# Optimization experiments

Hardware: AMD Instinct MI355X
Metric: run time of the kernel (lower is better)

The kernel has to match this reference:

```python
import jax, jax.numpy as jnp
import numpy as np

N = 100000   # nodes
E = 1600000  # edges (avg degree 16)
G = 512      # graphs in batch
IN = 96      # in_channels
H = 128      # hidden_channels
C = 100      # num_classes
ED = 8       # edge_dim
L = 4        # num_layers
EPS_LN = 1e-5


def setup_inputs() -> dict:
    key = jax.random.key(0)
    ks = jax.random.split(key, 24)
    s = 0.05
    d = {
        "x": jax.random.normal(ks[0], (N, IN), jnp.float32),
        "edge_index": jax.random.randint(ks[1], (2, E), 0, N, jnp.int32),
        "batch": jnp.sort(jax.random.randint(ks[2], (N,), 0, G, jnp.int32)),
        "edge_attr": jax.random.normal(ks[3], (E, ED), jnp.float32),
        # edge encoder MLP: Linear(ED,H) -> ReLU -> Linear(H,1)
        "ee_W1": jax.random.normal(ks[4], (ED, H), jnp.float32) * s,
        "ee_b1": jnp.zeros((H,), jnp.float32),
        "ee_W2": jax.random.normal(ks[5], (H, 1), jnp.float32) * s,
        "ee_b2": jnp.zeros((1,), jnp.float32),
        # GCNConv weights (PyG: lin without bias, bias added after aggregation)
        "W0": jax.random.normal(ks[6], (IN, H), jnp.float32) * s,
        "cb0": jnp.zeros((H,), jnp.float32),
        "W1": jax.random.normal(ks[7], (H, H), jnp.float32) * s,
        "cb1": jnp.zeros((H,), jnp.float32),
        "W2": jax.random.normal(ks[8], (H, H), jnp.float32) * s,
        "cb2": jnp.zeros((H,), jnp.float32),
        "W3": jax.random.normal(ks[9], (H, H), jnp.float32) * s,
        "cb3": jnp.zeros((H,), jnp.float32),
        # LayerNorm params
        "g0": jnp.ones((H,), jnp.float32), "be0": jnp.zeros((H,), jnp.float32),
        "g1": jnp.ones((H,), jnp.float32), "be1": jnp.zeros((H,), jnp.float32),
        "g2": jnp.ones((H,), jnp.float32), "be2": jnp.zeros((H,), jnp.float32),
        "g3": jnp.ones((H,), jnp.float32), "be3": jnp.zeros((H,), jnp.float32),
        # residual projection for layer 0 only (IN != H)
        "res_W": jax.random.normal(ks[10], (IN, H), jnp.float32) * s,
        "res_b": jnp.zeros((H,), jnp.float32),
        # head: Linear(2H,H) -> ReLU -> Linear(H,C)
        "hW1": jax.random.normal(ks[11], (2 * H, H), jnp.float32) * s,
        "hb1": jnp.zeros((H,), jnp.float32),
        "hW2": jax.random.normal(ks[12], (H, C), jnp.float32) * s,
        "hb2": jnp.zeros((C,), jnp.float32),
    }
    return d


def _layer_norm(h, g, b):
    mu = jnp.mean(h, axis=-1, keepdims=True)
    var = jnp.mean(jnp.square(h - mu), axis=-1, keepdims=True)
    return g * (h - mu) / jnp.sqrt(var + EPS_LN) + b


def reference(x, edge_index, batch, edge_attr,
              ee_W1, ee_b1, ee_W2, ee_b2,
              W0, cb0, W1, cb1, W2, cb2, W3, cb3,
              g0, be0, g1, be1, g2, be2, g3, be3,
              res_W, res_b, hW1, hb1, hW2, hb2):
    row, col = edge_index[0], edge_index[1]

    # edge weight = softplus(MLP(edge_attr)) + 1e-4  -> [E]
    eh = jax.nn.relu(edge_attr @ ee_W1 + ee_b1)
    ew = jax.nn.softplus((eh @ ee_W2 + ee_b2)[:, 0]) + 1e-4

    # add self loops with weight 1 (PyG GCNConv default)
    loops = jnp.arange(N, dtype=row.dtype)
    row_sl = jnp.concatenate([row, loops])
    col_sl = jnp.concatenate([col, loops])
    ew_sl = jnp.concatenate([ew, jnp.ones((N,), ew.dtype)])

    # symmetric normalization: D^-1/2 A D^-1/2 (deg over target index)
    deg = jax.ops.segment_sum(ew_sl, col_sl, num_segments=N)
    dis = jnp.where(deg > 0, jax.lax.rsqrt(deg), 0.0)
    norm = dis[row_sl] * ew_sl * dis[col_sl]  # [E+N]

    def conv(h, W, b):
        hw = h @ W                                   # [N,H]
        msg = hw[row_sl] * norm[:, None]             # [E+N,H]
        return jax.ops.segment_sum(msg, col_sl, num_segments=N) + b

    Ws = [W0, W1, W2, W3]
    cbs = [cb0, cb1, cb2, cb3]
    gs = [g0, g1, g2, g3]
    bes = [be0, be1, be2, be3]

    hidden = []
    cur = x
    for i in range(L):
        h = conv(cur, Ws[i], cbs[i])
        h = _layer_norm(h, gs[i], bes[i])
        res = cur @ res_W + res_b if i == 0 else cur
        h = jax.nn.relu(h + res)
        # dropout: eval mode -> identity
        hidden.append(h)
        cur = h
    xm = jnp.mean(jnp.stack(hidden, axis=0), axis=0)  # [N,H]

    # meanmax pooling over graphs
    counts = jax.ops.segment_sum(jnp.ones((N,), xm.dtype), batch, num_segments=G)
    gmean = jax.ops.segment_sum(xm, batch, num_segments=G) / jnp.maximum(counts, 1.0)[:, None]
    gmax = jax.ops.segment_max(xm, batch, num_segments=G)
    gmax = jnp.where(jnp.isfinite(gmax), gmax, 0.0)
    g = jnp.concatenate([gmean, gmax], axis=-1)       # [G,2H]

    # head (dropout identity in eval)
    return jax.nn.relu(g @ hW1 + hb1) @ hW2 + hb2     # [G,C]
```

## Files before the change

### kernel.cpp

```cpp
#include <hip/hip_runtime.h>
#include <hip/hip_fp16.h>
#include <math.h>

#define NN 100000
#define EE 1600000
#define GB 512
#define INC 96
#define HH 128
#define CC 100
#define MAXD 64
#define BUCKB 9
#define NBUK 196
#define CAPB 10240
#define EB 4096

typedef __bf16 bf16x8 __attribute__((ext_vector_type(8)));
typedef _Float16 f16x8 __attribute__((ext_vector_type(8)));
typedef float f32x4 __attribute__((ext_vector_type(4)));

__device__ __forceinline__ float unpack_w_f32(unsigned v) {
    return __half2float(__ushort_as_half((unsigned short)(v & 0x7FFFu)));
}
__device__ __forceinline__ __half2 unpack_w_h2(unsigned v) {
    __half h = __ushort_as_half((unsigned short)(v & 0x7FFFu));
    return __halves2half2(h, h);
}

__global__ __launch_bounds__(256) void k_cast(const float* __restrict__ src, __half* __restrict__ dst, int n4) {
    int i = blockIdx.x * 256 + threadIdx.x;
    if (i >= n4) return;
    float4 v = *(const float4*)&src[(size_t)i * 4];
    __half2 a = __floats2half2_rn(v.x, v.y);
    __half2 b = __floats2half2_rn(v.z, v.w);
    *(__half2*)&dst[(size_t)i * 4]     = a;
    *(__half2*)&dst[(size_t)i * 4 + 2] = b;
}

__global__ __launch_bounds__(256) void k_prep_weights(
    const float* __restrict__ W0, const float* __restrict__ resW,
    const float* __restrict__ W1m, const float* __restrict__ W2m, const float* __restrict__ W3m,
    __half* __restrict__ wt0, __half* __restrict__ wtR,
    __half* __restrict__ wt1, __half* __restrict__ wt2, __half* __restrict__ wt3)
{
    int idx = blockIdx.x * 256 + threadIdx.x;
    const float* src; __half* dst; int K, base;
    if (idx < 12288)      { src = W0;   dst = wt0; K = 96;  base = 0; }
    else if (idx < 24576) { src = resW; dst = wtR; K = 96;  base = 12288; }
    else if (idx < 40960) { src = W1m;  dst = wt1; K = 128; base = 24576; }
    else if (idx < 57344) { src = W2m;  dst = wt2; K = 128; base = 40960; }
    else if (idx < 73728) { src = W3m;  dst = wt3; K = 128; base = 57344; }
    else return;
    int l = idx - base;
    int k = l >> 7, n = l & 127;
    dst[(size_t)n * K + k] = __float2half(src[l]);
}

__global__ __launch_bounds__(512) void k_prep_w1(const float* __restrict__ W1, __bf16* __restrict__ w1f) {
    int tid = threadIdx.x;
    int t = tid >> 6, lane = tid & 63;
    int ln15 = lane & 15, quad = lane >> 4;
    bf16x8 v = {};
    if (quad == 0) {
#pragma unroll
        for (int j = 0; j < 8; ++j) v[j] = (__bf16)W1[j * 128 + t * 16 + ln15];
    }
    *(bf16x8*)&w1f[(size_t)(t * 64 + lane) * 8] = v;
}

__global__ __launch_bounds__(256) void k_edge_mlp_mfma(
    const float* __restrict__ ea,
    const __bf16* __restrict__ w1f, const float* __restrict__ b1,
    const float* __restrict__ W2, const float* __restrict__ b2,
    __half* __restrict__ ew)
{
    __shared__ float sDot[128];
    int tid = threadIdx.x, wva = tid >> 6, lane = tid & 63;
    int ln15 = lane & 15, quad = lane >> 4;
    int ebase = blockIdx.x * 128 + wva * 32;

    bf16x8 bfr[8];
#pragma unroll
    for (int t = 0; t < 8; ++t) bfr[t] = *(const bf16x8*)&w1f[(size_t)(t * 64 + lane) * 8];

    bf16x8 a0 = {}, a1 = {};
    if (quad == 0) {
        const float* p0 = &ea[(size_t)(ebase + ln15) * 8];
        float4 u0 = *(const float4*)p0, u1 = *(const float4*)(p0 + 4);
        a0[0] = (__bf16)u0.x; a0[1] = (__bf16)u0.y; a0[2] = (__bf16)u0.z; a0[3] = (__bf16)u0.w;
        a0[4] = (__bf16)u1.x; a0[5] = (__bf16)u1.y; a0[6] = (__bf16)u1.z; a0[7] = (__bf16)u1.w;
        const float* p1 = &ea[(size_t)(ebase + 16 + ln15) * 8];
        float4 w0 = *(const float4*)p1, w1v = *(const float4*)(p1 + 4);
        a1[0] = (__bf16)w0.x; a1[1] = (__bf16)w0.y; a1[2] = (__bf16)w0.z; a1[3] = (__bf16)w0.w;
        a1[4] = (__bf16)w1v.x; a1[5] = (__bf16)w1v.y; a1[6] = (__bf16)w1v.z; a1[7] = (__bf16)w1v.w;
    }

    f32x4 d0 = {0.f, 0.f, 0.f, 0.f}, d1 = {0.f, 0.f, 0.f, 0.f};
#pragma unroll
    for (int t = 0; t < 8; ++t) {
        f32x4 z = {0.f, 0.f, 0.f, 0.f};
        f32x4 c0 = __builtin_amdgcn_mfma_f32_16x16x32_bf16(a0, bfr[t], z, 0, 0, 0);
        f32x4 c1 = __builtin_amdgcn_mfma_f32_16x16x32_bf16(a1, bfr[t], z, 0, 0, 0);
        int col = t * 16 + ln15;
        float b1v = b1[col], w2v = W2[col];
#pragma unroll
        for (int r = 0; r < 4; ++r) {
            float v0 = fmaxf(c0[r] + b1v, 0.0f);
            float v1 = fmaxf(c1[r] + b1v, 0.0f);
            d0[r] = fmaf(v0, w2v, d0[r]);
            d1[r] = fmaf(v1, w2v, d1[r]);
        }
    }
#pragma unroll
    for (int o = 1; o < 16; o <<= 1) {
#pragma unroll
        for (int r = 0; r < 4; ++r) {
            d0[r] += __shfl_xor(d0[r], o, 64);
            d1[r] += __shfl_xor(d1[r], o, 64);
        }
    }
    if (ln15 == 0) {
#pragma unroll
        for (int r = 0; r < 4; ++r) {
            sDot[wva * 32 + quad * 4 + r]      = d0[r];
            sDot[wva * 32 + 16 + quad * 4 + r] = d1[r];
        }
    }
    __syncthreads();
    if (tid < 128) {
        int e = blockIdx.x * 128 + tid;
        float x = sDot[tid] + b2[0];
        float sp = (x > 20.0f) ? x : log1pf(expf(x));
        ew[e] = __float2half(sp + 1e-4f);
    }
}

__global__ __launch_bounds__(256) void k_split(const int* __restrict__ ei, const __half* __restrict__ ew,
                                               int* __restrict__ cntB, uint2* __restrict__ barr) {
    __shared__ unsigned hist[NBUK];
    __shared__ unsigned gbase[NBUK];
    __shared__ unsigned short rloc[EB];
    int tid = threadIdx.x;
    for (int b = tid; b < NBUK; b += 256) hist[b] = 0;
    __syncthreads();
    int e0 = blockIdx.x * EB;
#pragma unroll
    for (int j = 0; j < EB / 256; ++j) {
        int e = e0 + j * 256 + tid;
        if (e < EE) {
            int c = ei[EE + e];
            rloc[j * 256 + tid] = (unsigned short)atomicAdd(&hist[c >> BUCKB], 1u);
        }
    }
    __syncthreads();
    for (int b = tid; b < NBUK; b += 256)
        gbase[b] = (hist[b] > 0) ? (unsigned)atomicAdd(&cntB[b], (int)hist[b]) : 0u;
    __syncthreads();
#pragma unroll
    for (int j = 0; j < EB / 256; ++j) {
        int e = e0 + j * 256 + tid;
        if (e < EE) {
            int c = ei[EE + e];
            int b = c >> BUCKB;
            unsigned pos = gbase[b] + rloc[j * 256 + tid];
            if (pos < CAPB) {
                unsigned hb = (unsigned)__half_as_ushort(ew[e]) & 0x7FFFu;
                barr[(size_t)b * CAPB + pos] = make_uint2(((unsigned)c << 15) | hb, (unsigned)ei[e]);
            }
        }
    }
}

__global__ __launch_bounds__(256) void k_build(const int* __restrict__ cntB, const uint2* __restrict__ barr,
                                               unsigned* __restrict__ epack, int* __restrict__ cnt,
                                               float* __restrict__ dis) {
    __shared__ unsigned ncnt[512];
    __shared__ float ndeg[512];
    int tid = threadIdx.x, b = blockIdx.x;
    for (int i = tid; i < 512; i += 256) { ncnt[i] = 0; ndeg[i] = 0.0f; }
    __syncthreads();
    int n0 = b << BUCKB;
    int m = cntB[b]; if (m > CAPB) m = CAPB;
    for (int i = tid; i < m; i += 256) {
        uint2 rec = barr[(size_t)b * CAPB + i];
        int c = (int)(rec.x >> 15);
        int cl = c - n0;
        unsigned rank = atomicAdd(&ncnt[cl], 1u);
        if (rank < MAXD) epack[(size_t)c * MAXD + rank] = (rec.y << 15) | (rec.x & 0x7FFFu);
        atomicAdd(&ndeg[cl], unpack_w_f32(rec.x));
    }
    __syncthreads();
    int nn = NN - n0; if (nn > 512) nn = 512;
    for (int i = tid; i < nn; i += 256) {
        unsigned cc = ncnt[i]; if (cc > MAXD) cc = MAXD;
        cnt[n0 + i] = (int)cc;
        dis[n0 + i] = rsqrtf(1.0f + ndeg[i]);
    }
}

__global__ __launch_bounds__(256) void k_norm(const int* __restrict__ cnt, const float* __restrict__ dis,
                                              unsigned* __restrict__ epack, int n) {
    int wv = threadIdx.x >> 6, lane = threadIdx.x & 63;
    int i = blockIdx.x * 4 + wv;
    if (i >= n) return;
    float dc = dis[i];
    if (lane < cnt[i]) {
        unsigned v = epack[(size_t)i * MAXD + lane];
        float wn = dis[v >> 15] * unpack_w_f32(v) * dc;
        unsigned hb = (unsigned)__half_as_ushort(__float2half(wn)) & 0x7FFFu;
        epack[(size_t)i * MAXD + lane] = (v & 0xFFFF8000u) | hb;
    }
}

__global__ __launch_bounds__(256) void k_gemm_f16(
    const __half* __restrict__ A, const __half* __restrict__ Bt,
    const float* __restrict__ bias, __half* __restrict__ C, int M, int K)
{
    int tid = threadIdx.x;
    int wv = tid >> 6, lane = tid & 63;
    int ln15 = lane & 15, quad = lane >> 4;
    int m0 = blockIdx.x * 64;
    int n0 = wv * 32;
    f32x4 acc[4][2];
#pragma unroll
    for (int mt = 0; mt < 4; ++mt)
#pragma unroll
        for (int nt = 0; nt < 2; ++nt) acc[mt][nt] = (f32x4){0.f, 0.f, 0.f, 0.f};

    int rowm[4];
#pragma unroll
    for (int mt = 0; mt < 4; ++mt) {
        int r = m0 + mt * 16 + ln15;
        rowm[mt] = r < M ? r : M - 1;
    }
    for (int kc = 0; kc < K; kc += 32) {
        f16x8 af[4], bfr[2];
#pragma unroll
        for (int mt = 0; mt < 4; ++mt)
            af[mt] = *(const f16x8*)&A[(size_t)rowm[mt] * K + kc + quad * 8];
#pragma unroll
        for (int nt = 0; nt < 2; ++nt)
            bfr[nt] = *(const f16x8*)&Bt[(size_t)(n0 + nt * 16 + ln15) * K + kc + quad * 8];
#pragma unroll
        for (int mt = 0; mt < 4; ++mt)
#pragma unroll
            for (int nt = 0; nt < 2; ++nt)
                acc[mt][nt] = __builtin_amdgcn_mfma_f32_16x16x32_f16(af[mt], bfr[nt], acc[mt][nt], 0, 0, 0);
    }
#pragma unroll
    for (int nt = 0; nt < 2; ++nt) {
        int col = n0 + nt * 16 + ln15;
        float bv = bias ? bias[col] : 0.0f;
#pragma unroll
        for (int mt = 0; mt < 4; ++mt) {
#pragma unroll
            for (int r = 0; r < 4; ++r) {
                int row = m0 + mt * 16 + quad * 4 + r;
                if (row < M) C[(size_t)row * 128 + col] = __float2half(acc[mt][nt][r] + bv);
            }
        }
    }
}

__global__ __launch_bounds__(256) void k_agg_ln(
    const __half* __restrict__ hw, const float* __restrict__ dis,
    const int* __restrict__ cnt, const unsigned* __restrict__ epack,
    const float* __restrict__ cb, const float* __restrict__ gam,
    const float* __restrict__ bet, const __half* __restrict__ res,
    __half* __restrict__ out, int n)
{
    int wv = threadIdx.x >> 6;
    int lane = threadIdx.x & 63;
    int i = blockIdx.x * 4 + wv;
    if (i >= n) return;
    float di = dis[i];
    float sn = di * di;
    __half2 own = *(const __half2*)&hw[(size_t)i * HH + lane * 2];
    __half hsn = __float2half(sn);
    __half2 acc = __hmul2(own, __halves2half2(hsn, hsn));
    int cn = cnt[i];
    const unsigned* ebase = &epack[(size_t)i * MAXD];
    int k = 0;
    for (; k + 8 <= cn; k += 8) {
        uint4 q0 = *(const uint4*)&ebase[k];
        uint4 q1 = *(const uint4*)&ebase[k + 4];
        __half2 v0 = *(const __half2*)&hw[(size_t)(q0.x >> 15) * HH + lane * 2];
        __half2 v1 = *(const __half2*)&hw[(size_t)(q0.y >> 15) * HH + lane * 2];
        __half2 v2 = *(const __half2*)&hw[(size_t)(q0.z >> 15) * HH + lane * 2];
        __half2 v3 = *(const __half2*)&hw[(size_t)(q0.w >> 15) * HH + lane * 2];
        __half2 v4 = *(const __half2*)&hw[(size_t)(q1.x >> 15) * HH + lane * 2];
        __half2 v5 = *(const __half2*)&hw[(size_t)(q1.y >> 15) * HH + lane * 2];
        __half2 v6 = *(const __half2*)&hw[(size_t)(q1.z >> 15) * HH + lane * 2];
        __half2 v7 = *(const __half2*)&hw[(size_t)(q1.w >> 15) * HH + lane * 2];
        acc = __hfma2(v0, unpack_w_h2(q0.x), acc);
        acc = __hfma2(v1, unpack_w_h2(q0.y), acc);
        acc = __hfma2(v2, unpack_w_h2(q0.z), acc);
        acc = __hfma2(v3, unpack_w_h2(q0.w), acc);
        acc = __hfma2(v4, unpack_w_h2(q1.x), acc);
        acc = __hfma2(v5, unpack_w_h2(q1.y), acc);
        acc = __hfma2(v6, unpack_w_h2(q1.z), acc);
        acc = __hfma2(v7, unpack_w_h2(q1.w), acc);
    }
    for (; k < cn; ++k) {
        unsigned e = ebase[k];
        __half2 v = *(const __half2*)&hw[(size_t)(e >> 15) * HH + lane * 2];
        acc = __hfma2(v, unpack_w_h2(e), acc);
    }
    float2 af = __half22float2(acc);
    float2 cbv = *(const float2*)&cb[lane * 2];
    af.x += cbv.x; af.y += cbv.y;
    float s1 = af.x + af.y;
    float s2 = af.x * af.x + af.y * af.y;
#pragma unroll
    for (int o = 32; o > 0; o >>= 1) {
        s1 += __shfl_xor(s1, o, 64);
        s2 += __shfl_xor(s2, o, 64);
    }
    float mean = s1 * (1.0f / HH);
    float var = fmaxf(s2 * (1.0f / HH) - mean * mean, 0.0f);
    float rstd = rsqrtf(var + 1e-5f);
    float2 gv = *(const float2*)&gam[lane * 2];
    float2 bv = *(const float2*)&bet[lane * 2];
    float2 rv = __half22float2(*(const __half2*)&res[(size_t)i * HH + lane * 2]);
    float hx = fmaxf(fmaf(gv.x, (af.x - mean) * rstd, bv.x) + rv.x, 0.0f);
    float hy = fmaxf(fmaf(gv.y, (af.y - mean) * rstd, bv.y) + rv.y, 0.0f);
    *(__half2*)&out[(size_t)i * HH + lane * 2] = __floats2half2_rn(hx, hy);
}

__global__ __launch_bounds__(512) void k_pool(
    const __half* __restrict__ l0, const __half* __restrict__ l1,
    const __half* __restrict__ l2, const __half* __restrict__ l3,
    const int* __restrict__ batch, float* __restrict__ gbuf, int n)
{
    __shared__ float ssum[8][128];
    __shared__ float smax[8][128];
    int g = blockIdx.x, tid = threadIdx.x;
    int grp = tid >> 6, lane = tid & 63;
    int lo = 0, hi = n;
    while (lo < hi) { int m = (lo + hi) >> 1; if (batch[m] < g) lo = m + 1; else hi = m; }
    int start = lo;
    lo = start; hi = n;
    while (lo < hi) { int m = (lo + hi) >> 1; if (batch[m] < g + 1) lo = m + 1; else hi = m; }
    int end = lo;
    float sx = 0.0f, sy = 0.0f, mx = -INFINITY, my = -INFINITY;
    for (int nd = start + grp; nd < end; nd += 8) {
        size_t off = (size_t)nd * HH + lane * 2;
        float2 v0 = __half22float2(*(const __half2*)&l0[off]);
        float2 v1 = __half22float2(*(const __half2*)&l1[off]);
        float2 v2 = __half22float2(*(const __half2*)&l2[off]);
        float2 v3 = __half22float2(*(const __half2*)&l3[off]);
        float vx = (v0.x + v1.x + v2.x + v3.x) * 0.25f;
        float vy = (v0.y + v1.y + v2.y + v3.y) * 0.25f;
        sx += vx; sy += vy;
        mx = fmaxf(mx, vx); my = fmaxf(my, vy);
    }
    ssum[grp][lane * 2] = sx; ssum[grp][lane * 2 + 1] = sy;
    smax[grp][lane * 2] = mx; smax[grp][lane * 2 + 1] = my;
    __syncthreads();
    if (tid < 128) {
        float s = 0.0f, m = -INFINITY;
#pragma unroll
        for (int j = 0; j < 8; ++j) {
            s += ssum[j][tid];
            m = fmaxf(m, smax[j][tid]);
        }
        int cntg = end - start;
        gbuf[(size_t)g * 256 + tid] = s / fmaxf((float)cntg, 1.0f);
        gbuf[(size_t)g * 256 + 128 + tid] = (cntg > 0) ? m : 0.0f;
    }
}

__global__ __launch_bounds__(128) void k_head(const float* __restrict__ gbuf,
                                              const float* __restrict__ hW1, const float* __restrict__ hb1,
                                              const float* __restrict__ hW2, const float* __restrict__ hb2,
                                              float* __restrict__ out) {
    __shared__ __align__(16) float sg[256];
    __shared__ __align__(16) float sh[128];
    int g = blockIdx.x, t = threadIdx.x;
    sg[t] = gbuf[(size_t)g * 256 + t];
    sg[t + 128] = gbuf[(size_t)g * 256 + 128 + t];
    __syncthreads();
    float h = hb1[t];
    for (int k = 0; k < 256; ++k) h = fmaf(sg[k], hW1[(size_t)k * 128 + t], h);
    sh[t] = fmaxf(h, 0.0f);
    __syncthreads();
    if (t < 100) {
        float o = hb2[t];
        for (int k = 0; k < 128; ++k) o = fmaf(sh[k], hW2[(size_t)k * 100 + t], o);
        out[(size_t)g * 100 + t] = o;
    }
}

extern "C" void kernel_launch(void* const* d_in, const int* in_sizes, int n_in,
                              void* d_out, int out_size, void* d_ws, size_t ws_size,
                              hipStream_t stream) {
    const float* x     = (const float*)d_in[0];
    const int*   ei    = (const int*)d_in[1];
    const int*   batch = (const int*)d_in[2];
    const float* ea    = (const float*)d_in[3];
    const float* eeW1  = (const float*)d_in[4];
    const float* eeb1  = (const float*)d_in[5];
    const float* eeW2  = (const float*)d_in[6];
    const float* eeb2  = (const float*)d_in[7];
    const float* W[4]  = {(const float*)d_in[8], (const float*)d_in[10], (const float*)d_in[12], (const float*)d_in[14]};
    const float* cb[4] = {(const float*)d_in[9], (const float*)d_in[11], (const float*)d_in[13], (const float*)d_in[15]};
    const float* gm[4] = {(const float*)d_in[16], (const float*)d_in[18], (const float*)d_in[20], (const float*)d_in[22]};
    const float* be[4] = {(const float*)d_in[17], (const float*)d_in[19], (const float*)d_in[21], (const float*)d_in[23]};
    const float* resW  = (const float*)d_in[24];
    const float* resb  = (const float*)d_in[25];
    const float* hW1   = (const float*)d_in[26];
    const float* hb1   = (const float*)d_in[27];
    const float* hW2   = (const float*)d_in[28];
    const float* hb2   = (const float*)d_in[29];
    float* out = (float*)d_out;

    char* w = (char*)d_ws;
    auto alloc = [&](size_t bytes) { void* p = w; w += (bytes + 255) & ~(size_t)255; return p; };
    __half*   ew     = (__half*)  alloc((size_t)EE * 2);
    float*    dis    = (float*)   alloc((size_t)NN * 4);
    int*      cnt    = (int*)     alloc((size_t)NN * 4);
    int*      cntB   = (int*)     alloc((size_t)NBUK * 4);
    uint2*    barr   = (uint2*)   alloc((size_t)NBUK * CAPB * 8);
    unsigned* epack  = (unsigned*)alloc((size_t)NN * MAXD * 4);
    __half*   xb     = (__half*)  alloc((size_t)NN * INC * 2);
    __half*   hw     = (__half*)  alloc((size_t)NN * HH * 2);
    __half*   lout[4];
    for (int i = 0; i < 4; ++i) lout[i] = (__half*)alloc((size_t)NN * HH * 2);
    float*    gbuf   = (float*)   alloc((size_t)GB * 256 * 4);
    __half*   wt0    = (__half*)  alloc((size_t)INC * HH * 2);
    __half*   wtR    = (__half*)  alloc((size_t)INC * HH * 2);
    __half*   wt1    = (__half*)  alloc((size_t)HH * HH * 2);
    __half*   wt2    = (__half*)  alloc((size_t)HH * HH * 2);
    __half*   wt3    = (__half*)  alloc((size_t)HH * HH * 2);
    __bf16*   w1f    = (__bf16*)  alloc((size_t)8 * 64 * 8 * 2);
    __half*   wtc[4] = {wt0, wt1, wt2, wt3};
    __half*   res0   = lout[1];

    int nblkEdge = EE / 128;
    int nblkSplit = (EE + EB - 1) / EB;
    int nblkGemm = (NN + 63) / 64;
    int nblkCast = (NN * INC / 4 + 255) / 256;

    hipMemsetAsync(cntB, 0, (size_t)NBUK * 4, stream);
    k_cast<<<nblkCast, 256, 0, stream>>>(x, xb, NN * INC / 4);
    k_prep_weights<<<288, 256, 0, stream>>>(W[0], resW, W[1], W[2], W[3], wt0, wtR, wt1, wt2, wt3);
    k_prep_w1<<<1, 512, 0, stream>>>(eeW1, w1f);
    k_edge_mlp_mfma<<<nblkEdge, 256, 0, stream>>>(ea, w1f, eeb1, eeW2, eeb2, ew);
    k_split<<<nblkSplit, 256, 0, stream>>>(ei, ew, cntB, barr);
    k_build<<<NBUK, 256, 0, stream>>>(cntB, barr, epack, cnt, dis);
    k_norm<<<(NN + 3) / 4, 256, 0, stream>>>(cnt, dis, epack, NN);

    k_gemm_f16<<<nblkGemm, 256, 0, stream>>>(xb, wt0, nullptr, hw, NN, INC);
    k_gemm_f16<<<nblkGemm, 256, 0, stream>>>(xb, wtR, resb, res0, NN, INC);
    k_agg_ln<<<(NN + 3) / 4, 256, 0, stream>>>(hw, dis, cnt, epack,
                                               cb[0], gm[0], be[0], res0, lout[0], NN);
    for (int l = 1; l < 4; ++l) {
        k_gemm_f16<<<nblkGemm, 256, 0, stream>>>(lout[l - 1], wtc[l], nullptr, hw, NN, HH);
        k_agg_ln<<<(NN + 3) / 4, 256, 0, stream>>>(hw, dis, cnt, epack,
                                                   cb[l], gm[l], be[l], lout[l - 1], lout[l], NN);
    }

    k_pool<<<GB, 512, 0, stream>>>(lout[0], lout[1], lout[2], lout[3], batch, gbuf, NN);
    k_head<<<GB, 128, 0, stream>>>(gbuf, hW1, hb1, hW2, hb2, out);
}
```

Measured before the change: 774.2 us.

## Fuse prep, dual layer-0 GEMMs, pool+head; split agg accumulators

```diff
diff --git a/kernel.cpp b/kernel.cpp
--- a/kernel.cpp
+++ b/kernel.cpp
@@ -36,13 +36,28 @@
     *(__half2*)&dst[(size_t)i * 4 + 2] = b;
 }
 
-__global__ __launch_bounds__(256) void k_prep_weights(
+__global__ __launch_bounds__(512) void k_prep(
     const float* __restrict__ W0, const float* __restrict__ resW,
     const float* __restrict__ W1m, const float* __restrict__ W2m, const float* __restrict__ W3m,
+    const float* __restrict__ eeW1,
     __half* __restrict__ wt0, __half* __restrict__ wtR,
-    __half* __restrict__ wt1, __half* __restrict__ wt2, __half* __restrict__ wt3)
+    __half* __restrict__ wt1, __half* __restrict__ wt2, __half* __restrict__ wt3,
+    __bf16* __restrict__ w1f)
 {
-    int idx = blockIdx.x * 256 + threadIdx.x;
+    int tid = threadIdx.x;
+    if (blockIdx.x == 288) {
+        int t = tid >> 6, lane = tid & 63;
+        int ln15 = lane & 15, quad = lane >> 4;
+        bf16x8 v = {};
+        if (quad == 0) {
+#pragma unroll
+            for (int j = 0; j < 8; ++j) v[j] = (__bf16)eeW1[j * 128 + t * 16 + ln15];
+        }
+        *(bf16x8*)&w1f[(size_t)(t * 64 + lane) * 8] = v;
+        return;
+    }
+    if (tid >= 256) return;
+    int idx = blockIdx.x * 256 + tid;
     const float* src; __half* dst; int K, base;
     if (idx < 12288)      { src = W0;   dst = wt0; K = 96;  base = 0; }
     else if (idx < 24576) { src = resW; dst = wtR; K = 96;  base = 12288; }
@@ -53,18 +68,6 @@
     int l = idx - base;
     int k = l >> 7, n = l & 127;
     dst[(size_t)n * K + k] = __float2half(src[l]);
-}
-
-__global__ __launch_bounds__(512) void k_prep_w1(const float* __restrict__ W1, __bf16* __restrict__ w1f) {
-    int tid = threadIdx.x;
-    int t = tid >> 6, lane = tid & 63;
-    int ln15 = lane & 15, quad = lane >> 4;
-    bf16x8 v = {};
-    if (quad == 0) {
-#pragma unroll
-        for (int j = 0; j < 8; ++j) v[j] = (__bf16)W1[j * 128 + t * 16 + ln15];
-    }
-    *(bf16x8*)&w1f[(size_t)(t * 64 + lane) * 8] = v;
 }
 
 __global__ __launch_bounds__(256) void k_edge_mlp_mfma(
@@ -256,6 +259,65 @@
             for (int r = 0; r < 4; ++r) {
                 int row = m0 + mt * 16 + quad * 4 + r;
                 if (row < M) C[(size_t)row * 128 + col] = __float2half(acc[mt][nt][r] + bv);
+            }
+        }
+    }
+}
+
+__global__ __launch_bounds__(256) void k_gemm_dual(
+    const __half* __restrict__ A, const __half* __restrict__ Bt1, const __half* __restrict__ Bt2,
+    const float* __restrict__ bias2, __half* __restrict__ C1, __half* __restrict__ C2, int M, int K)
+{
+    int tid = threadIdx.x;
+    int wv = tid >> 6, lane = tid & 63;
+    int ln15 = lane & 15, quad = lane >> 4;
+    int m0 = blockIdx.x * 64;
+    int n0 = wv * 32;
+    f32x4 acc1[4][2], acc2[4][2];
+#pragma unroll
+    for (int mt = 0; mt < 4; ++mt)
+#pragma unroll
+        for (int nt = 0; nt < 2; ++nt) {
+            acc1[mt][nt] = (f32x4){0.f, 0.f, 0.f, 0.f};
+            acc2[mt][nt] = (f32x4){0.f, 0.f, 0.f, 0.f};
+        }
+    int rowm[4];
+#pragma unroll
+    for (int mt = 0; mt < 4; ++mt) {
+        int r = m0 + mt * 16 + ln15;
+        rowm[mt] = r < M ? r : M - 1;
+    }
+    for (int kc = 0; kc < K; kc += 32) {
+        f16x8 af[4], bf1[2], bf2[2];
+#pragma unroll
+        for (int mt = 0; mt < 4; ++mt)
+            af[mt] = *(const f16x8*)&A[(size_t)rowm[mt] * K + kc + quad * 8];
+#pragma unroll
+        for (int nt = 0; nt < 2; ++nt) {
+            bf1[nt] = *(const f16x8*)&Bt1[(size_t)(n0 + nt * 16 + ln15) * K + kc + quad * 8];
+            bf2[nt] = *(const f16x8*)&Bt2[(size_t)(n0 + nt * 16 + ln15) * K + kc + quad * 8];
+        }
+#pragma unroll
+        for (int mt = 0; mt < 4; ++mt)
+#pragma unroll
+            for (int nt = 0; nt < 2; ++nt) {
+                acc1[mt][nt] = __builtin_amdgcn_mfma_f32_16x16x32_f16(af[mt], bf1[nt], acc1[mt][nt], 0, 0, 0);
+                acc2[mt][nt] = __builtin_amdgcn_mfma_f32_16x16x32_f16(af[mt], bf2[nt], acc2[mt][nt], 0, 0, 0);
+            }
+    }
+#pragma unroll
+    for (int nt = 0; nt < 2; ++nt) {
+        int col = n0 + nt * 16 + ln15;
+        float bv2 = bias2[col];
+#pragma unroll
+        for (int mt = 0; mt < 4; ++mt) {
+#pragma unroll
+            for (int r = 0; r < 4; ++r) {
+                int row = m0 + mt * 16 + quad * 4 + r;
+                if (row < M) {
+                    C1[(size_t)row * 128 + col] = __float2half(acc1[mt][nt][r]);
+                    C2[(size_t)row * 128 + col] = __float2half(acc2[mt][nt][r] + bv2);
+                }
             }
         }
     }
@@ -276,7 +338,8 @@
     float sn = di * di;
     __half2 own = *(const __half2*)&hw[(size_t)i * HH + lane * 2];
     __half hsn = __float2half(sn);
-    __half2 acc = __hmul2(own, __halves2half2(hsn, hsn));
+    __half2 acca = __hmul2(own, __halves2half2(hsn, hsn));
+    __half2 accb = __halves2half2(__float2half(0.0f), __float2half(0.0f));
     int cn = cnt[i];
     const unsigned* ebase = &epack[(size_t)i * MAXD];
     int k = 0;
@@ -291,20 +354,21 @@
         __half2 v5 = *(const __half2*)&hw[(size_t)(q1.y >> 15) * HH + lane * 2];
         __half2 v6 = *(const __half2*)&hw[(size_t)(q1.z >> 15) * HH + lane * 2];
         __half2 v7 = *(const __half2*)&hw[(size_t)(q1.w >> 15) * HH + lane * 2];
-        acc = __hfma2(v0, unpack_w_h2(q0.x), acc);
-        acc = __hfma2(v1, unpack_w_h2(q0.y), acc);
-        acc = __hfma2(v2, unpack_w_h2(q0.z), acc);
-        acc = __hfma2(v3, unpack_w_h2(q0.w), acc);
-        acc = __hfma2(v4, unpack_w_h2(q1.x), acc);
-        acc = __hfma2(v5, unpack_w_h2(q1.y), acc);
-        acc = __hfma2(v6, unpack_w_h2(q1.z), acc);
-        acc = __hfma2(v7, unpack_w_h2(q1.w), acc);
+        acca = __hfma2(v0, unpack_w_h2(q0.x), acca);
+        accb = __hfma2(v4, unpack_w_h2(q1.x), accb);
+        acca = __hfma2(v1, unpack_w_h2(q0.y), acca);
+        accb = __hfma2(v5, unpack_w_h2(q1.y), accb);
+        acca = __hfma2(v2, unpack_w_h2(q0.z), acca);
+        accb = __hfma2(v6, unpack_w_h2(q1.z), accb);
+        acca = __hfma2(v3, unpack_w_h2(q0.w), acca);
+        accb = __hfma2(v7, unpack_w_h2(q1.w), accb);
     }
     for (; k < cn; ++k) {
         unsigned e = ebase[k];
         __half2 v = *(const __half2*)&hw[(size_t)(e >> 15) * HH + lane * 2];
-        acc = __hfma2(v, unpack_w_h2(e), acc);
-    }
+        acca = __hfma2(v, unpack_w_h2(e), acca);
+    }
+    __half2 acc = __hadd2(acca, accb);
     float2 af = __half22float2(acc);
     float2 cbv = *(const float2*)&cb[lane * 2];
     af.x += cbv.x; af.y += cbv.y;
@@ -326,13 +390,18 @@
     *(__half2*)&out[(size_t)i * HH + lane * 2] = __floats2half2_rn(hx, hy);
 }
 
-__global__ __launch_bounds__(512) void k_pool(
+__global__ __launch_bounds__(512) void k_pool_head(
     const __half* __restrict__ l0, const __half* __restrict__ l1,
     const __half* __restrict__ l2, const __half* __restrict__ l3,
-    const int* __restrict__ batch, float* __restrict__ gbuf, int n)
+    const int* __restrict__ batch,
+    const float* __restrict__ hW1, const float* __restrict__ hb1,
+    const float* __restrict__ hW2, const float* __restrict__ hb2,
+    float* __restrict__ out, int n)
 {
     __shared__ float ssum[8][128];
     __shared__ float smax[8][128];
+    __shared__ __align__(16) float sg[256];
+    __shared__ __align__(16) float sh[128];
     int g = blockIdx.x, tid = threadIdx.x;
     int grp = tid >> 6, lane = tid & 63;
     int lo = 0, hi = n;
@@ -364,29 +433,20 @@
             m = fmaxf(m, smax[j][tid]);
         }
         int cntg = end - start;
-        gbuf[(size_t)g * 256 + tid] = s / fmaxf((float)cntg, 1.0f);
-        gbuf[(size_t)g * 256 + 128 + tid] = (cntg > 0) ? m : 0.0f;
-    }
-}
-
-__global__ __launch_bounds__(128) void k_head(const float* __restrict__ gbuf,
-                                              const float* __restrict__ hW1, const float* __restrict__ hb1,
-                                              const float* __restrict__ hW2, const float* __restrict__ hb2,
-                                              float* __restrict__ out) {
-    __shared__ __align__(16) float sg[256];
-    __shared__ __align__(16) float sh[128];
-    int g = blockIdx.x, t = threadIdx.x;
-    sg[t] = gbuf[(size_t)g * 256 + t];
-    sg[t + 128] = gbuf[(size_t)g * 256 + 128 + t];
-    __syncthreads();
-    float h = hb1[t];
-    for (int k = 0; k < 256; ++k) h = fmaf(sg[k], hW1[(size_t)k * 128 + t], h);
-    sh[t] = fmaxf(h, 0.0f);
-    __syncthreads();
-    if (t < 100) {
-        float o = hb2[t];
-        for (int k = 0; k < 128; ++k) o = fmaf(sh[k], hW2[(size_t)k * 100 + t], o);
-        out[(size_t)g * 100 + t] = o;
+        sg[tid] = s / fmaxf((float)cntg, 1.0f);
+        sg[128 + tid] = (cntg > 0) ? m : 0.0f;
+    }
+    __syncthreads();
+    if (tid < 128) {
+        float h = hb1[tid];
+        for (int k = 0; k < 256; ++k) h = fmaf(sg[k], hW1[(size_t)k * 128 + tid], h);
+        sh[tid] = fmaxf(h, 0.0f);
+    }
+    __syncthreads();
+    if (tid < 100) {
+        float o = hb2[tid];
+        for (int k = 0; k < 128; ++k) o = fmaf(sh[k], hW2[(size_t)k * 100 + tid], o);
+        out[(size_t)g * 100 + tid] = o;
     }
 }
 
@@ -420,12 +480,11 @@
     int*      cnt    = (int*)     alloc((size_t)NN * 4);
     int*      cntB   = (int*)     alloc((size_t)NBUK * 4);
     uint2*    barr   = (uint2*)   alloc((size_t)NBUK * CAPB * 8);
-    unsigned* epack  = (unsigned*)alloc((size_t)NN * MAXD * 4);
+    unsigned* epack  = (unsigned*)alloc((size_t)(NN * MAXD + 64) * 4);
     __half*   xb     = (__half*)  alloc((size_t)NN * INC * 2);
     __half*   hw     = (__half*)  alloc((size_t)NN * HH * 2);
     __half*   lout[4];
     for (int i = 0; i < 4; ++i) lout[i] = (__half*)alloc((size_t)NN * HH * 2);
-    float*    gbuf   = (float*)   alloc((size_t)GB * 256 * 4);
     __half*   wt0    = (__half*)  alloc((size_t)INC * HH * 2);
     __half*   wtR    = (__half*)  alloc((size_t)INC * HH * 2);
     __half*   wt1    = (__half*)  alloc((size_t)HH * HH * 2);
@@ -442,15 +501,14 @@
 
     hipMemsetAsync(cntB, 0, (size_t)NBUK * 4, stream);
     k_cast<<<nblkCast, 256, 0, stream>>>(x, xb, NN * INC / 4);
-    k_prep_weights<<<288, 256, 0, stream>>>(W[0], resW, W[1], W[2], W[3], wt0, wtR, wt1, wt2, wt3);
-    k_prep_w1<<<1, 512, 0, stream>>>(eeW1, w1f);
+    k_prep<<<289, 512, 0, stream>>>(W[0], resW, W[1], W[2], W[3], eeW1,
+                                    wt0, wtR, wt1, wt2, wt3, w1f);
     k_edge_mlp_mfma<<<nblkEdge, 256, 0, stream>>>(ea, w1f, eeb1, eeW2, eeb2, ew);
     k_split<<<nblkSplit, 256, 0, stream>>>(ei, ew, cntB, barr);
     k_build<<<NBUK, 256, 0, stream>>>(cntB, barr, epack, cnt, dis);
     k_norm<<<(NN + 3) / 4, 256, 0, stream>>>(cnt, dis, epack, NN);
 
-    k_gemm_f16<<<nblkGemm, 256, 0, stream>>>(xb, wt0, nullptr, hw, NN, INC);
-    k_gemm_f16<<<nblkGemm, 256, 0, stream>>>(xb, wtR, resb, res0, NN, INC);
+    k_gemm_dual<<<nblkGemm, 256, 0, stream>>>(xb, wt0, wtR, resb, hw, res0, NN, INC);
     k_agg_ln<<<(NN + 3) / 4, 256, 0, stream>>>(hw, dis, cnt, epack,
                                                cb[0], gm[0], be[0], res0, lout[0], NN);
     for (int l = 1; l < 4; ++l) {
@@ -459,6 +517,6 @@
                                                    cb[l], gm[l], be[l], lout[l - 1], lout[l], NN);
     }
 
-    k_pool<<<GB, 512, 0, stream>>>(lout[0], lout[1], lout[2], lout[3], batch, gbuf, NN);
-    k_head<<<GB, 128, 0, stream>>>(gbuf, hW1, hb1, hW2, hb2, out);
-}
+    k_pool_head<<<GB, 512, 0, stream>>>(lout[0], lout[1], lout[2], lout[3], batch,
+                                        hW1, hb1, hW2, hb2, out, NN);
+}
```

New measurement: 754.2 us. -2.6%, faster.
